# Optimization experiments

Measured on AMD Instinct MI355X. Metric: run time of the kernel, lower is better.

## Reference

```python
import jax, jax.numpy as jnp
import numpy as np

N = 50000      # nodes
E = 800000     # edges (avg degree 16)
DIN = 500      # input_dim
HID = 100      # hid_dim (fixed in module)
DOUT = 64      # output_dim
EPS = 1e-5     # LayerNorm eps (torch default)


def _layer_norm(x, g, b):
    mu = jnp.mean(x, axis=-1, keepdims=True)
    var = jnp.var(x, axis=-1, keepdims=True)
    return (x - mu) / jnp.sqrt(var + EPS) * g + b


def _gcn_conv(x, src, tgt, W, b):
    # PyG GCNConv: self-loops + symmetric normalization + linear + scatter-add
    h = x @ W  # [N, out]
    idx = jnp.arange(N)
    src_sl = jnp.concatenate([src, idx])
    tgt_sl = jnp.concatenate([tgt, idx])
    deg = jax.ops.segment_sum(jnp.ones(src_sl.shape, h.dtype), tgt_sl, num_segments=N)
    dinv = jnp.where(deg > 0, deg ** -0.5, 0.0)
    norm = dinv[src_sl] * dinv[tgt_sl]  # [E+N]
    out = jax.ops.segment_sum(h[src_sl] * norm[:, None], tgt_sl, num_segments=N)
    return out + b


def setup_inputs() -> dict:
    key = jax.random.key(0)
    ks = jax.random.split(key, 10)
    glorot = lambda k, fi, fo: jax.random.normal(k, (fi, fo), jnp.float32) * np.float32(1.0 / np.sqrt(fi))
    z = lambda d: jnp.zeros((d,), jnp.float32)
    return dict(
        data_x=jax.random.normal(ks[0], (N, DIN), jnp.float32),
        data_edge_index=jax.random.randint(ks[1], (2, E), 0, N),
        data_edge_attr=jnp.zeros((E,), jnp.int32),  # single relation type
        t_W1=glorot(ks[2], DIN, HID), t_b1=z(HID), t_g1=jnp.ones((HID,), jnp.float32), t_be1=z(HID),
        t_W2=glorot(ks[3], HID, HID), t_b2=z(HID), t_g2=jnp.ones((HID,), jnp.float32), t_be2=z(HID),
        r_Wrel=glorot(ks[4], HID, HID)[None],  # [n_relations=1, H, H]
        r_Wself=glorot(ks[5], HID, HID), r_b=z(HID),
        c1_W=glorot(ks[6], HID, HID), c1_b=z(HID),
        c2_W=glorot(ks[7], HID, DOUT), c2_b=z(DOUT),
    )


def reference(data_x, data_edge_index, data_edge_attr,
              t_W1, t_b1, t_g1, t_be1, t_W2, t_b2, t_g2, t_be2,
              r_Wrel, r_Wself, r_b, c1_W, c1_b, c2_W, c2_b):
    src, tgt = data_edge_index[0], data_edge_index[1]
    # transform: Linear -> LN -> ReLU -> Linear -> LN -> ReLU
    x = jax.nn.relu(_layer_norm(data_x @ t_W1 + t_b1, t_g1, t_be1))
    x = jax.nn.relu(_layer_norm(x @ t_W2 + t_b2, t_g2, t_be2))
    # RGCN, n_relations=1, n_layers=1: per-relation message + self transform
    msgs = x[src] @ r_Wrel[0]  # edge_attr is all relation 0
    x = x @ r_Wself + jax.ops.segment_sum(msgs, tgt, num_segments=N) + r_b
    x = jax.nn.relu(x)  # dropout = identity (eval)
    x = jax.nn.relu(_gcn_conv(x, src, tgt, c1_W, c1_b))
    x = _gcn_conv(x, src, tgt, c2_W, c2_b)
    return jax.nn.log_softmax(x, axis=1)
```

## Files before the change

kernel.cpp:

```cpp
#include <hip/hip_runtime.h>
#include <hip/hip_bf16.h>

typedef __attribute__((ext_vector_type(8))) short short8;
typedef __attribute__((ext_vector_type(8))) unsigned short ushort8;
typedef __attribute__((ext_vector_type(4))) float f32x4;

static constexpr int NN = 50000;
static constexpr int NE = 800000;
static constexpr int SCAN_B = 196;

#define MFMA16x16x32 __builtin_amdgcn_mfma_f32_16x16x32_bf16

__device__ __forceinline__ float b2f(unsigned short u){
  unsigned v = ((unsigned)u) << 16;
  return __builtin_bit_cast(float, v);
}
__device__ __forceinline__ unsigned short f2b(float f){
  unsigned x = __builtin_bit_cast(unsigned, f);
  unsigned r = (x + 0x7fffu + ((x >> 16) & 1u)) >> 16;
  return (unsigned short)r;
}

__device__ __align__(256) int   g_isf32;
__device__ __align__(256) unsigned short g_W1t  [112 * 512];
__device__ __align__(256) unsigned short g_W2t  [112 * 128];
__device__ __align__(256) unsigned short g_WselfT[112 * 128];
__device__ __align__(256) unsigned short g_WrelT [112 * 128];
__device__ __align__(256) unsigned short g_c1Wt [112 * 128];
__device__ __align__(256) unsigned short g_c2Wt [64 * 128];
__device__ __align__(256) unsigned short g_bufA[(size_t)NN * 128];
__device__ __align__(256) unsigned short g_bufB[(size_t)NN * 128];
__device__ __align__(256) unsigned short g_bufC[(size_t)NN * 128];
__device__ __align__(256) int   g_deg[NN];
__device__ __align__(256) int   g_rowptr[NN + 1];
__device__ __align__(256) int   g_cursor[NN];
__device__ __align__(256) int   g_colidx[NE];
__device__ __align__(256) float g_dinv[NN];
__device__ __align__(256) int   g_partial[256];

__device__ __forceinline__ float ld_in(const void* p, int idx, int isf32){
  if (isf32) return ((const float*)p)[idx];
  return b2f(((const unsigned short*)p)[idx]);
}

__global__ void k_detect(const unsigned short* __restrict__ x){
  __shared__ int sh[256];
  int tid = threadIdx.x;
  int cnt = 0;
  for (int j = 0; j < 16; j++){
    unsigned short h = x[(size_t)(tid * 16 + j) * 2];
    int e = (h >> 7) & 0xFF;
    if (e >= 90 && e <= 160) cnt++;
  }
  sh[tid] = cnt;
  __syncthreads();
  for (int off = 128; off > 0; off >>= 1){
    if (tid < off) sh[tid] += sh[tid + off];
    __syncthreads();
  }
  if (tid == 0) g_isf32 = (sh[0] < 2458) ? 1 : 0;
}

__global__ void k_zero(){
  int i = blockIdx.x * 256 + threadIdx.x;
  if (i < NN){ g_deg[i] = 0; g_cursor[i] = 0; }
}

__device__ __forceinline__ void xp_one(const void* W, unsigned short* Wt, int idx,
                                       int K, int Nc, int Kpad, int isf32){
  int n = idx / Kpad;
  int k = idx - n * Kpad;
  float v = 0.f;
  if (n < Nc && k < K) v = ld_in(W, k * Nc + n, isf32);
  Wt[idx] = f2b(v);
}
__global__ void k_transpose_all(const void* W1, const void* W2, const void* Wself,
                                const void* Wrel, const void* c1W, const void* c2W){
  int idx = blockIdx.x * 256 + threadIdx.x;
  const int isf32 = g_isf32;
  if (idx < 57344){ xp_one(W1, g_W1t, idx, 500, 100, 512, isf32); return; }
  idx -= 57344;
  if (idx < 14336){ xp_one(W2,    g_W2t,    idx, 100, 100, 128, isf32); return; }
  idx -= 14336;
  if (idx < 14336){ xp_one(Wself, g_WselfT, idx, 100, 100, 128, isf32); return; }
  idx -= 14336;
  if (idx < 14336){ xp_one(Wrel,  g_WrelT,  idx, 100, 100, 128, isf32); return; }
  idx -= 14336;
  if (idx < 14336){ xp_one(c1W,   g_c1Wt,   idx, 100, 100, 128, isf32); return; }
  idx -= 14336;
  if (idx < 8192){  xp_one(c2W,   g_c2Wt,   idx, 100, 64,  128, isf32); }
}

__global__ void k_deg(const int* __restrict__ tgt){
  int e = blockIdx.x * 256 + threadIdx.x;
  if (e < NE) atomicAdd(&g_deg[tgt[e]], 1);
}

__global__ __launch_bounds__(256) void k_scan1(){
  __shared__ int sh[256];
  int t = threadIdx.x;
  int i = blockIdx.x * 256 + t;
  int val = (i < NN) ? g_deg[i] : 0;
  sh[t] = val;
  __syncthreads();
#pragma unroll
  for (int off = 1; off < 256; off <<= 1){
    int v = (t >= off) ? sh[t - off] : 0;
    __syncthreads();
    sh[t] += v;
    __syncthreads();
  }
  if (i < NN){
    g_rowptr[i] = sh[t] - val;
    g_dinv[i] = rsqrtf((float)(val + 1));
  }
  if (t == 255) g_partial[blockIdx.x] = sh[255];
}
__global__ __launch_bounds__(256) void k_scan2(){
  __shared__ int sh[256];
  int t = threadIdx.x;
  int val = (t < SCAN_B) ? g_partial[t] : 0;
  sh[t] = val;
  __syncthreads();
#pragma unroll
  for (int off = 1; off < 256; off <<= 1){
    int v = (t >= off) ? sh[t - off] : 0;
    __syncthreads();
    sh[t] += v;
    __syncthreads();
  }
  if (t < SCAN_B) g_partial[t] = sh[t] - val;
  if (t == 255) g_rowptr[NN] = sh[255];
}
__global__ __launch_bounds__(256) void k_scan3(){
  int i = blockIdx.x * 256 + threadIdx.x;
  if (i < NN) g_rowptr[i] += g_partial[blockIdx.x];
}

__global__ void k_fill(const int* __restrict__ src, const int* __restrict__ tgt){
  int e = blockIdx.x * 256 + threadIdx.x;
  if (e >= NE) return;
  int t = tgt[e];
  int pos = g_rowptr[t] + atomicAdd(&g_cursor[t], 1);
  g_colidx[pos] = src[e];
}

template<int MODE>
__global__ __launch_bounds__(256) void k_agg(){
  const unsigned short* x = (MODE == 1) ? g_bufC : g_bufB;
  int node = blockIdx.x * 16 + (threadIdx.x >> 4);
  if (node >= NN) return;
  const int c8 = (threadIdx.x & 15) * 8;

  float wt = (MODE != 0) ? g_dinv[node] : 1.f;
  float a[4][8];
#pragma unroll
  for (int j = 0; j < 4; j++)
#pragma unroll
    for (int k = 0; k < 8; k++) a[j][k] = 0.f;

  int p0 = g_rowptr[node], p1 = g_rowptr[node + 1];
  for (int p = p0; p < p1; p += 4){
    int   sj[4]; float wj[4];
#pragma unroll
    for (int j = 0; j < 4; j++){
      bool ok = (p + j) < p1;
      sj[j] = ok ? g_colidx[p + j] : node;
      wj[j] = ok ? ((MODE != 0) ? g_dinv[sj[j]] * wt : 1.f) : 0.f;
    }
    ushort8 r[4];
#pragma unroll
    for (int j = 0; j < 4; j++)
      r[j] = *reinterpret_cast<const ushort8*>(&x[(size_t)sj[j] * 128 + c8]);
#pragma unroll
    for (int j = 0; j < 4; j++)
#pragma unroll
      for (int k = 0; k < 8; k++) a[j][k] += wj[j] * b2f((unsigned short)r[j][k]);
  }
  if (MODE != 0){
    float ws = wt * wt;
    ushort8 sv = *reinterpret_cast<const ushort8*>(&x[(size_t)node * 128 + c8]);
#pragma unroll
    for (int k = 0; k < 8; k++) a[0][k] += ws * b2f((unsigned short)sv[k]);
  }
  ushort8 o;
#pragma unroll
  for (int k = 0; k < 8; k++)
    o[k] = f2b(a[0][k] + a[1][k] + a[2][k] + a[3][k]);
  *reinterpret_cast<ushort8*>(&g_bufA[(size_t)node * 128 + c8]) = o;
}

__global__ __launch_bounds__(256, 4) void k_gemm1_ln(const void* __restrict__ Aext,
    const void* __restrict__ bias, const void* __restrict__ gamma,
    const void* __restrict__ beta){
  __shared__ float red[28 * 256];
  const int tid = threadIdx.x;
  const int w = tid >> 6, lane = tid & 63;
  const int m = lane & 15, q = lane >> 4;
  const int row0 = blockIdx.x * 16;
  const int isf32 = g_isf32;
  const int kbase = w * 128;
  f32x4 acc[7] = {};

  if (isf32){
    const float* base = (const float*)Aext + (size_t)(row0 + m) * 500;
    f32x4 L[8];
#pragma unroll
    for (int c = 0; c < 4; c++){
      int col = kbase + c * 32 + q * 8;
      L[2 * c]     = *reinterpret_cast<const f32x4*>(base + min(col, 496));
      L[2 * c + 1] = *reinterpret_cast<const f32x4*>(base + min(col + 4, 496));
    }
#pragma unroll
    for (int c = 0; c < 4; c++){
      f32x4 lo = L[2 * c], hi = L[2 * c + 1];
      short8 a = {(short)f2b(lo[0]), (short)f2b(lo[1]), (short)f2b(lo[2]), (short)f2b(lo[3]),
                  (short)f2b(hi[0]), (short)f2b(hi[1]), (short)f2b(hi[2]), (short)f2b(hi[3])};
      const int k0 = kbase + c * 32 + q * 8;
#pragma unroll
      for (int t = 0; t < 7; t++){
        short8 b = *reinterpret_cast<const short8*>(g_W1t + (size_t)(t * 16 + m) * 512 + k0);
        acc[t] = MFMA16x16x32(a, b, acc[t], 0, 0, 0);
      }
    }
  } else {
    const unsigned short* base = (const unsigned short*)Aext + (size_t)(row0 + m) * 500;
    ushort4 U[8];
#pragma unroll
    for (int c = 0; c < 4; c++){
      int col = kbase + c * 32 + q * 8;
      U[2 * c]     = *reinterpret_cast<const ushort4*>(base + min(col, 496));
      U[2 * c + 1] = *reinterpret_cast<const ushort4*>(base + min(col + 4, 496));
    }
#pragma unroll
    for (int c = 0; c < 4; c++){
      ushort4 lo = U[2 * c], hi = U[2 * c + 1];
      short8 a = {(short)lo.x, (short)lo.y, (short)lo.z, (short)lo.w,
                  (short)hi.x, (short)hi.y, (short)hi.z, (short)hi.w};
      const int k0 = kbase + c * 32 + q * 8;
#pragma unroll
      for (int t = 0; t < 7; t++){
        short8 b = *reinterpret_cast<const short8*>(g_W1t + (size_t)(t * 16 + m) * 512 + k0);
        acc[t] = MFMA16x16x32(a, b, acc[t], 0, 0, 0);
      }
    }
  }

#pragma unroll
  for (int t = 0; t < 7; t++)
#pragma unroll
    for (int r = 0; r < 4; r++)
      red[(t * 4 + r) * 256 + tid] = acc[t][r];
  __syncthreads();
  if (w != 0) return;

  float bf_[7], gf_[7], ef_[7];
#pragma unroll
  for (int t = 0; t < 7; t++){
    int col = t * 16 + m;
    bool ok = col < 100;
    bf_[t] = ok ? ld_in(bias, col, isf32)  : 0.f;
    gf_[t] = ok ? ld_in(gamma, col, isf32) : 0.f;
    ef_[t] = ok ? ld_in(beta, col, isf32)  : 0.f;
  }
#pragma unroll
  for (int r = 0; r < 4; r++){
    float vals[7], s1 = 0.f, s2 = 0.f;
#pragma unroll
    for (int t = 0; t < 7; t++){
      const float* rv = &red[(t * 4 + r) * 256];
      float v = rv[lane] + rv[64 + lane] + rv[128 + lane] + rv[192 + lane];
      int col = t * 16 + m;
      v = (col < 100) ? (v + bf_[t]) : 0.f;
      vals[t] = v; s1 += v; s2 += v * v;
    }
#pragma unroll
    for (int msk = 1; msk < 16; msk <<= 1){
      s1 += __shfl_xor(s1, msk, 64);
      s2 += __shfl_xor(s2, msk, 64);
    }
    float mu = s1 * 0.01f;
    float var = fmaxf(s2 * 0.01f - mu * mu, 0.f);
    float rstd = rsqrtf(var + 1e-5f);
    unsigned short* orow = g_bufA + (size_t)(row0 + q * 4 + r) * 128;
#pragma unroll
    for (int t = 0; t < 7; t++){
      int col = t * 16 + m;
      float y = fmaxf((vals[t] - mu) * rstd * gf_[t] + ef_[t], 0.f);
      orow[col] = f2b((col < 100) ? y : 0.f);
    }
    orow[112 + m] = 0;
  }
}

__global__ __launch_bounds__(256) void k_gemm2_ln(const void* __restrict__ bias,
    const void* __restrict__ gamma, const void* __restrict__ beta){
  const int isf32 = g_isf32;
  const int wave = threadIdx.x >> 6, lane = threadIdx.x & 63;
  const int m = lane & 15, q = lane >> 4;
  const int row0 = (blockIdx.x * 4 + wave) * 16;
  if (row0 >= NN) return;
  f32x4 acc[7] = {};
  const unsigned short* arow = g_bufA + (size_t)(row0 + m) * 128;
#pragma unroll
  for (int c = 0; c < 4; c++){
    const int k0 = c * 32 + q * 8;
    short8 a = *reinterpret_cast<const short8*>(arow + k0);
#pragma unroll
    for (int t = 0; t < 7; t++){
      short8 b = *reinterpret_cast<const short8*>(g_W2t + (size_t)(t * 16 + m) * 128 + k0);
      acc[t] = MFMA16x16x32(a, b, acc[t], 0, 0, 0);
    }
  }
  float bf_[7], gf_[7], ef_[7];
#pragma unroll
  for (int t = 0; t < 7; t++){
    int col = t * 16 + m;
    bool ok = col < 100;
    bf_[t] = ok ? ld_in(bias, col, isf32)  : 0.f;
    gf_[t] = ok ? ld_in(gamma, col, isf32) : 0.f;
    ef_[t] = ok ? ld_in(beta, col, isf32)  : 0.f;
  }
#pragma unroll
  for (int r = 0; r < 4; r++){
    float vals[7], s1 = 0.f, s2 = 0.f;
#pragma unroll
    for (int t = 0; t < 7; t++){
      int col = t * 16 + m;
      float v = (col < 100) ? (acc[t][r] + bf_[t]) : 0.f;
      vals[t] = v; s1 += v; s2 += v * v;
    }
#pragma unroll
    for (int msk = 1; msk < 16; msk <<= 1){
      s1 += __shfl_xor(s1, msk, 64);
      s2 += __shfl_xor(s2, msk, 64);
    }
    float mu = s1 * 0.01f;
    float var = fmaxf(s2 * 0.01f - mu * mu, 0.f);
    float rstd = rsqrtf(var + 1e-5f);
    unsigned short* orow = g_bufB + (size_t)(row0 + q * 4 + r) * 128;
#pragma unroll
    for (int t = 0; t < 7; t++){
      int col = t * 16 + m;
      float y = fmaxf((vals[t] - mu) * rstd * gf_[t] + ef_[t], 0.f);
      orow[col] = f2b((col < 100) ? y : 0.f);
    }
    orow[112 + m] = 0;
  }
}

template<int SEL>
__global__ __launch_bounds__(256) void k_gemm_bias_relu(const void* __restrict__ bias){
  const unsigned short* A1  = (SEL == 0) ? g_bufB : g_bufA;
  const unsigned short* B1t = (SEL == 0) ? g_WselfT : g_c1Wt;
  unsigned short* out       = (SEL == 0) ? g_bufC : g_bufB;
  const int isf32 = g_isf32;

  const int wave = threadIdx.x >> 6, lane = threadIdx.x & 63;
  const int m = lane & 15, q = lane >> 4;
  const int row0 = (blockIdx.x * 4 + wave) * 16;
  if (row0 >= NN) return;
  f32x4 acc[7] = {};
  const unsigned short* a1row = A1 + (size_t)(row0 + m) * 128;
#pragma unroll
  for (int c = 0; c < 4; c++){
    const int k0 = c * 32 + q * 8;
    short8 a = *reinterpret_cast<const short8*>(a1row + k0);
#pragma unroll
    for (int t = 0; t < 7; t++){
      short8 b = *reinterpret_cast<const short8*>(B1t + (size_t)(t * 16 + m) * 128 + k0);
      acc[t] = MFMA16x16x32(a, b, acc[t], 0, 0, 0);
    }
  }
  if (SEL == 0){
    const unsigned short* a2row = g_bufA + (size_t)(row0 + m) * 128;
#pragma unroll
    for (int c = 0; c < 4; c++){
      const int k0 = c * 32 + q * 8;
      short8 a = *reinterpret_cast<const short8*>(a2row + k0);
#pragma unroll
      for (int t = 0; t < 7; t++){
        short8 b = *reinterpret_cast<const short8*>(g_WrelT + (size_t)(t * 16 + m) * 128 + k0);
        acc[t] = MFMA16x16x32(a, b, acc[t], 0, 0, 0);
      }
    }
  }
  float bf_[7];
#pragma unroll
  for (int t = 0; t < 7; t++){
    int col = t * 16 + m;
    bf_[t] = (col < 100) ? ld_in(bias, col, isf32) : 0.f;
  }
#pragma unroll
  for (int r = 0; r < 4; r++){
    unsigned short* orow = out + (size_t)(row0 + q * 4 + r) * 128;
#pragma unroll
    for (int t = 0; t < 7; t++){
      int col = t * 16 + m;
      float y = fmaxf(acc[t][r] + bf_[t], 0.f);
      orow[col] = f2b((col < 100) ? y : 0.f);
    }
    orow[112 + m] = 0;
  }
}

__global__ __launch_bounds__(256) void k_gemm_c2(){
  const int wave = threadIdx.x >> 6, lane = threadIdx.x & 63;
  const int m = lane & 15, q = lane >> 4;
  const int row0 = (blockIdx.x * 4 + wave) * 16;
  if (row0 >= NN) return;
  f32x4 acc[4] = {};
  const unsigned short* arow = g_bufB + (size_t)(row0 + m) * 128;
#pragma unroll
  for (int c = 0; c < 4; c++){
    const int k0 = c * 32 + q * 8;
    short8 a = *reinterpret_cast<const short8*>(arow + k0);
#pragma unroll
    for (int t = 0; t < 4; t++){
      short8 b = *reinterpret_cast<const short8*>(g_c2Wt + (size_t)(t * 16 + m) * 128 + k0);
      acc[t] = MFMA16x16x32(a, b, acc[t], 0, 0, 0);
    }
  }
#pragma unroll
  for (int r = 0; r < 4; r++){
    unsigned short* orow = g_bufC + (size_t)(row0 + q * 4 + r) * 64;
#pragma unroll
    for (int t = 0; t < 4; t++) orow[t * 16 + m] = f2b(acc[t][r]);
  }
}

__global__ __launch_bounds__(256) void k_agg_lsm(const void* __restrict__ bias,
                                                 void* __restrict__ outv){
  const int isf32 = g_isf32;
  int node = blockIdx.x * 32 + (threadIdx.x >> 3);
  if (node >= NN) return;
  const int c8 = (threadIdx.x & 7) * 8;
  float wt = g_dinv[node];
  float a[4][8];
#pragma unroll
  for (int j = 0; j < 4; j++)
#pragma unroll
    for (int k = 0; k < 8; k++) a[j][k] = 0.f;

  int p0 = g_rowptr[node], p1 = g_rowptr[node + 1];
  for (int p = p0; p < p1; p += 4){
    int   sj[4]; float wj[4];
#pragma unroll
    for (int j = 0; j < 4; j++){
      bool ok = (p + j) < p1;
      sj[j] = ok ? g_colidx[p + j] : node;
      wj[j] = ok ? g_dinv[sj[j]] * wt : 0.f;
    }
    ushort8 r[4];
#pragma unroll
    for (int j = 0; j < 4; j++)
      r[j] = *reinterpret_cast<const ushort8*>(&g_bufC[(size_t)sj[j] * 64 + c8]);
#pragma unroll
    for (int j = 0; j < 4; j++)
#pragma unroll
      for (int k = 0; k < 8; k++) a[j][k] += wj[j] * b2f((unsigned short)r[j][k]);
  }
  float ws = wt * wt;
  ushort8 sv = *reinterpret_cast<const ushort8*>(&g_bufC[(size_t)node * 64 + c8]);
#pragma unroll
  for (int k = 0; k < 8; k++) a[0][k] += ws * b2f((unsigned short)sv[k]);

  float v[8], mx = -1e30f;
#pragma unroll
  for (int k = 0; k < 8; k++){
    v[k] = a[0][k] + a[1][k] + a[2][k] + a[3][k] + ld_in(bias, c8 + k, isf32);
    mx = fmaxf(mx, v[k]);
  }
#pragma unroll
  for (int msk = 1; msk < 8; msk <<= 1) mx = fmaxf(mx, __shfl_xor(mx, msk, 64));
  float se = 0.f;
#pragma unroll
  for (int k = 0; k < 8; k++) se += expf(v[k] - mx);
#pragma unroll
  for (int msk = 1; msk < 8; msk <<= 1) se += __shfl_xor(se, msk, 64);
  float lse = logf(se);
  size_t ro = (size_t)node * 64 + c8;
  if (isf32){
    float* o = (float*)outv + ro;
#pragma unroll
    for (int k = 0; k < 8; k++) o[k] = v[k] - mx - lse;
  } else {
    unsigned short* o = (unsigned short*)outv + ro;
#pragma unroll
    for (int k = 0; k < 8; k++) o[k] = f2b(v[k] - mx - lse);
  }
}

extern "C" void kernel_launch(void* const* d_in, const int* in_sizes, int n_in,
                              void* d_out, int out_size, void* d_ws, size_t ws_size,
                              hipStream_t stream){
  (void)in_sizes; (void)n_in; (void)out_size; (void)d_ws; (void)ws_size;
  const void* data_x = d_in[0];
  const int* ei = (const int*)d_in[1];
  const int* src = ei;
  const int* tgt = ei + NE;
  const void *W1 = d_in[3], *b1 = d_in[4], *gm1 = d_in[5], *be1 = d_in[6];
  const void *W2 = d_in[7], *b2 = d_in[8], *gm2 = d_in[9], *be2 = d_in[10];
  const void *Wrel = d_in[11], *Wself = d_in[12], *rb = d_in[13];
  const void *c1W = d_in[14], *c1b = d_in[15];
  const void *c2W = d_in[16], *c2b = d_in[17];

  k_detect<<<1, 256, 0, stream>>>((const unsigned short*)data_x);
  k_zero<<<(NN + 255) / 256, 256, 0, stream>>>();
  k_transpose_all<<<(122880 + 255) / 256, 256, 0, stream>>>(W1, W2, Wself, Wrel, c1W, c2W);

  k_deg<<<(NE + 255) / 256, 256, 0, stream>>>(tgt);
  k_scan1<<<SCAN_B, 256, 0, stream>>>();
  k_scan2<<<1, 256, 0, stream>>>();
  k_scan3<<<SCAN_B, 256, 0, stream>>>();
  k_fill<<<(NE + 255) / 256, 256, 0, stream>>>(src, tgt);

  const int G64 = (NN + 63) / 64;
  const int GA  = (NN + 15) / 16;
  k_gemm1_ln<<<3125, 256, 0, stream>>>(data_x, b1, gm1, be1);
  k_gemm2_ln<<<G64, 256, 0, stream>>>(b2, gm2, be2);
  k_agg<0><<<GA, 256, 0, stream>>>();
  k_gemm_bias_relu<0><<<G64, 256, 0, stream>>>(rb);
  k_agg<1><<<GA, 256, 0, stream>>>();
  k_gemm_bias_relu<1><<<G64, 256, 0, stream>>>(c1b);
  k_gemm_c2<<<G64, 256, 0, stream>>>();
  k_agg_lsm<<<(NN + 31) / 32, 256, 0, stream>>>(c2b, d_out);
}
```

Before: 507.1 us.

## Fuse aggregation and GEMM stages into shared-memory pipelines, merge detect and zero

Merges detect and zero into one launch. The first two dense layers now run in one kernel that keeps the intermediate in LDS, and each aggregation is fused with its following GEMM(s) through an LDS tile. This cuts kernel launches and removes global round-trips of the intermediate activations. In exchange the GEMM K dimension is split across four waves and reduced through a large shared buffer, and the gather-heavy aggregation now shares blocks with MFMA work, which may lower occupancy.

```diff
diff --git a/kernel.cpp b/kernel.cpp
--- a/kernel.cpp
+++ b/kernel.cpp
@@ -43,27 +43,27 @@
   return b2f(((const unsigned short*)p)[idx]);
 }
 
-__global__ void k_detect(const unsigned short* __restrict__ x){
-  __shared__ int sh[256];
-  int tid = threadIdx.x;
-  int cnt = 0;
-  for (int j = 0; j < 16; j++){
-    unsigned short h = x[(size_t)(tid * 16 + j) * 2];
-    int e = (h >> 7) & 0xFF;
-    if (e >= 90 && e <= 160) cnt++;
-  }
-  sh[tid] = cnt;
-  __syncthreads();
-  for (int off = 128; off > 0; off >>= 1){
-    if (tid < off) sh[tid] += sh[tid + off];
+__global__ void k_detect_zero(const unsigned short* __restrict__ x){
+  if (blockIdx.x == 0){
+    __shared__ int sh[256];
+    int tid = threadIdx.x;
+    int cnt = 0;
+    for (int j = 0; j < 16; j++){
+      unsigned short h = x[(size_t)(tid * 16 + j) * 2];
+      int e = (h >> 7) & 0xFF;
+      if (e >= 90 && e <= 160) cnt++;
+    }
+    sh[tid] = cnt;
     __syncthreads();
-  }
-  if (tid == 0) g_isf32 = (sh[0] < 2458) ? 1 : 0;
-}
-
-__global__ void k_zero(){
-  int i = blockIdx.x * 256 + threadIdx.x;
-  if (i < NN){ g_deg[i] = 0; g_cursor[i] = 0; }
+    for (int off = 128; off > 0; off >>= 1){
+      if (tid < off) sh[tid] += sh[tid + off];
+      __syncthreads();
+    }
+    if (tid == 0) g_isf32 = (sh[0] < 2458) ? 1 : 0;
+  } else {
+    int i = (blockIdx.x - 1) * 256 + threadIdx.x;
+    if (i < NN){ g_deg[i] = 0; g_cursor[i] = 0; }
+  }
 }
 
 __device__ __forceinline__ void xp_one(const void* W, unsigned short* Wt, int idx,
@@ -95,39 +95,29 @@
   int e = blockIdx.x * 256 + threadIdx.x;
   if (e < NE) atomicAdd(&g_deg[tgt[e]], 1);
 }
-
 __global__ __launch_bounds__(256) void k_scan1(){
   __shared__ int sh[256];
   int t = threadIdx.x;
   int i = blockIdx.x * 256 + t;
   int val = (i < NN) ? g_deg[i] : 0;
-  sh[t] = val;
-  __syncthreads();
+  sh[t] = val; __syncthreads();
 #pragma unroll
   for (int off = 1; off < 256; off <<= 1){
     int v = (t >= off) ? sh[t - off] : 0;
-    __syncthreads();
-    sh[t] += v;
-    __syncthreads();
-  }
-  if (i < NN){
-    g_rowptr[i] = sh[t] - val;
-    g_dinv[i] = rsqrtf((float)(val + 1));
-  }
+    __syncthreads(); sh[t] += v; __syncthreads();
+  }
+  if (i < NN){ g_rowptr[i] = sh[t] - val; g_dinv[i] = rsqrtf((float)(val + 1)); }
   if (t == 255) g_partial[blockIdx.x] = sh[255];
 }
 __global__ __launch_bounds__(256) void k_scan2(){
   __shared__ int sh[256];
   int t = threadIdx.x;
   int val = (t < SCAN_B) ? g_partial[t] : 0;
-  sh[t] = val;
-  __syncthreads();
+  sh[t] = val; __syncthreads();
 #pragma unroll
   for (int off = 1; off < 256; off <<= 1){
     int v = (t >= off) ? sh[t - off] : 0;
-    __syncthreads();
-    sh[t] += v;
-    __syncthreads();
+    __syncthreads(); sh[t] += v; __syncthreads();
   }
   if (t < SCAN_B) g_partial[t] = sh[t] - val;
   if (t == 255) g_rowptr[NN] = sh[255];
@@ -136,7 +126,6 @@
   int i = blockIdx.x * 256 + threadIdx.x;
   if (i < NN) g_rowptr[i] += g_partial[blockIdx.x];
 }
-
 __global__ void k_fill(const int* __restrict__ src, const int* __restrict__ tgt){
   int e = blockIdx.x * 256 + threadIdx.x;
   if (e >= NE) return;
@@ -145,63 +134,9 @@
   g_colidx[pos] = src[e];
 }
 
-template<int MODE>
-__global__ __launch_bounds__(256) void k_agg(){
-  const unsigned short* x = (MODE == 1) ? g_bufC : g_bufB;
-  int node = blockIdx.x * 16 + (threadIdx.x >> 4);
-  if (node >= NN) return;
-  const int c8 = (threadIdx.x & 15) * 8;
-
-  float wt = (MODE != 0) ? g_dinv[node] : 1.f;
-  float a[4][8];
-#pragma unroll
-  for (int j = 0; j < 4; j++)
-#pragma unroll
-    for (int k = 0; k < 8; k++) a[j][k] = 0.f;
-
-  int p0 = g_rowptr[node], p1 = g_rowptr[node + 1];
-  for (int p = p0; p < p1; p += 4){
-    int   sj[4]; float wj[4];
-#pragma unroll
-    for (int j = 0; j < 4; j++){
-      bool ok = (p + j) < p1;
-      sj[j] = ok ? g_colidx[p + j] : node;
-      wj[j] = ok ? ((MODE != 0) ? g_dinv[sj[j]] * wt : 1.f) : 0.f;
-    }
-    ushort8 r[4];
-#pragma unroll
-    for (int j = 0; j < 4; j++)
-      r[j] = *reinterpret_cast<const ushort8*>(&x[(size_t)sj[j] * 128 + c8]);
-#pragma unroll
-    for (int j = 0; j < 4; j++)
-#pragma unroll
-      for (int k = 0; k < 8; k++) a[j][k] += wj[j] * b2f((unsigned short)r[j][k]);
-  }
-  if (MODE != 0){
-    float ws = wt * wt;
-    ushort8 sv = *reinterpret_cast<const ushort8*>(&x[(size_t)node * 128 + c8]);
-#pragma unroll
-    for (int k = 0; k < 8; k++) a[0][k] += ws * b2f((unsigned short)sv[k]);
-  }
-  ushort8 o;
-#pragma unroll
-  for (int k = 0; k < 8; k++)
-    o[k] = f2b(a[0][k] + a[1][k] + a[2][k] + a[3][k]);
-  *reinterpret_cast<ushort8*>(&g_bufA[(size_t)node * 128 + c8]) = o;
-}
-
-__global__ __launch_bounds__(256, 4) void k_gemm1_ln(const void* __restrict__ Aext,
-    const void* __restrict__ bias, const void* __restrict__ gamma,
-    const void* __restrict__ beta){
-  __shared__ float red[28 * 256];
-  const int tid = threadIdx.x;
-  const int w = tid >> 6, lane = tid & 63;
-  const int m = lane & 15, q = lane >> 4;
-  const int row0 = blockIdx.x * 16;
-  const int isf32 = g_isf32;
-  const int kbase = w * 128;
-  f32x4 acc[7] = {};
-
+
+__device__ __forceinline__ void body_gemm1_compute(const void* Aext, int row0,
+    int m, int q, int kbase, int isf32, f32x4* acc){
   if (isf32){
     const float* base = (const float*)Aext + (size_t)(row0 + m) * 500;
     f32x4 L[8];
@@ -245,15 +180,18 @@
       }
     }
   }
-
-#pragma unroll
-  for (int t = 0; t < 7; t++)
-#pragma unroll
-    for (int r = 0; r < 4; r++)
-      red[(t * 4 + r) * 256 + tid] = acc[t][r];
-  __syncthreads();
-  if (w != 0) return;
-
+}
+
+__device__ __forceinline__ short8 frag_from_lds(const float* xT, int m, int k0){
+  const float* ax = xT + m * 132 + k0;
+  short8 a = {(short)f2b(ax[0]), (short)f2b(ax[1]), (short)f2b(ax[2]), (short)f2b(ax[3]),
+              (short)f2b(ax[4]), (short)f2b(ax[5]), (short)f2b(ax[6]), (short)f2b(ax[7])};
+  return a;
+}
+
+__device__ __forceinline__ void epi_ln_to_lds(const float* red, float* xT,
+    int lane, int m, int q, int isf32,
+    const void* bias, const void* gamma, const void* beta){
   float bf_[7], gf_[7], ef_[7];
 #pragma unroll
   for (int t = 0; t < 7; t++){
@@ -282,36 +220,20 @@
     float mu = s1 * 0.01f;
     float var = fmaxf(s2 * 0.01f - mu * mu, 0.f);
     float rstd = rsqrtf(var + 1e-5f);
-    unsigned short* orow = g_bufA + (size_t)(row0 + q * 4 + r) * 128;
+    float* xrow = xT + (q * 4 + r) * 132;
 #pragma unroll
     for (int t = 0; t < 7; t++){
       int col = t * 16 + m;
       float y = fmaxf((vals[t] - mu) * rstd * gf_[t] + ef_[t], 0.f);
-      orow[col] = f2b((col < 100) ? y : 0.f);
-    }
-    orow[112 + m] = 0;
-  }
-}
-
-__global__ __launch_bounds__(256) void k_gemm2_ln(const void* __restrict__ bias,
-    const void* __restrict__ gamma, const void* __restrict__ beta){
-  const int isf32 = g_isf32;
-  const int wave = threadIdx.x >> 6, lane = threadIdx.x & 63;
-  const int m = lane & 15, q = lane >> 4;
-  const int row0 = (blockIdx.x * 4 + wave) * 16;
-  if (row0 >= NN) return;
-  f32x4 acc[7] = {};
-  const unsigned short* arow = g_bufA + (size_t)(row0 + m) * 128;
-#pragma unroll
-  for (int c = 0; c < 4; c++){
-    const int k0 = c * 32 + q * 8;
-    short8 a = *reinterpret_cast<const short8*>(arow + k0);
-#pragma unroll
-    for (int t = 0; t < 7; t++){
-      short8 b = *reinterpret_cast<const short8*>(g_W2t + (size_t)(t * 16 + m) * 128 + k0);
-      acc[t] = MFMA16x16x32(a, b, acc[t], 0, 0, 0);
-    }
-  }
+      xrow[col] = (col < 100) ? y : 0.f;
+    }
+    xrow[112 + m] = 0.f;
+  }
+}
+
+__device__ __forceinline__ void epi_ln_to_global(const float* red, unsigned short* outb,
+    int row0, int lane, int m, int q, int isf32,
+    const void* bias, const void* gamma, const void* beta){
   float bf_[7], gf_[7], ef_[7];
 #pragma unroll
   for (int t = 0; t < 7; t++){
@@ -326,8 +248,10 @@
     float vals[7], s1 = 0.f, s2 = 0.f;
 #pragma unroll
     for (int t = 0; t < 7; t++){
+      const float* rv = &red[(t * 4 + r) * 256];
+      float v = rv[lane] + rv[64 + lane] + rv[128 + lane] + rv[192 + lane];
       int col = t * 16 + m;
-      float v = (col < 100) ? (acc[t][r] + bf_[t]) : 0.f;
+      v = (col < 100) ? (v + bf_[t]) : 0.f;
       vals[t] = v; s1 += v; s2 += v * v;
     }
 #pragma unroll
@@ -338,7 +262,7 @@
     float mu = s1 * 0.01f;
     float var = fmaxf(s2 * 0.01f - mu * mu, 0.f);
     float rstd = rsqrtf(var + 1e-5f);
-    unsigned short* orow = g_bufB + (size_t)(row0 + q * 4 + r) * 128;
+    unsigned short* orow = outb + (size_t)(row0 + q * 4 + r) * 128;
 #pragma unroll
     for (int t = 0; t < 7; t++){
       int col = t * 16 + m;
@@ -349,42 +273,9 @@
   }
 }
 
-template<int SEL>
-__global__ __launch_bounds__(256) void k_gemm_bias_relu(const void* __restrict__ bias){
-  const unsigned short* A1  = (SEL == 0) ? g_bufB : g_bufA;
-  const unsigned short* B1t = (SEL == 0) ? g_WselfT : g_c1Wt;
-  unsigned short* out       = (SEL == 0) ? g_bufC : g_bufB;
-  const int isf32 = g_isf32;
-
-  const int wave = threadIdx.x >> 6, lane = threadIdx.x & 63;
-  const int m = lane & 15, q = lane >> 4;
-  const int row0 = (blockIdx.x * 4 + wave) * 16;
-  if (row0 >= NN) return;
-  f32x4 acc[7] = {};
-  const unsigned short* a1row = A1 + (size_t)(row0 + m) * 128;
-#pragma unroll
-  for (int c = 0; c < 4; c++){
-    const int k0 = c * 32 + q * 8;
-    short8 a = *reinterpret_cast<const short8*>(a1row + k0);
-#pragma unroll
-    for (int t = 0; t < 7; t++){
-      short8 b = *reinterpret_cast<const short8*>(B1t + (size_t)(t * 16 + m) * 128 + k0);
-      acc[t] = MFMA16x16x32(a, b, acc[t], 0, 0, 0);
-    }
-  }
-  if (SEL == 0){
-    const unsigned short* a2row = g_bufA + (size_t)(row0 + m) * 128;
-#pragma unroll
-    for (int c = 0; c < 4; c++){
-      const int k0 = c * 32 + q * 8;
-      short8 a = *reinterpret_cast<const short8*>(a2row + k0);
-#pragma unroll
-      for (int t = 0; t < 7; t++){
-        short8 b = *reinterpret_cast<const short8*>(g_WrelT + (size_t)(t * 16 + m) * 128 + k0);
-        acc[t] = MFMA16x16x32(a, b, acc[t], 0, 0, 0);
-      }
-    }
-  }
+__device__ __forceinline__ void epi_biasrelu_to_global(const float* red,
+    unsigned short* outb, int row0, int lane, int m, int q, int isf32,
+    const void* bias){
   float bf_[7];
 #pragma unroll
   for (int t = 0; t < 7; t++){
@@ -393,39 +284,213 @@
   }
 #pragma unroll
   for (int r = 0; r < 4; r++){
-    unsigned short* orow = out + (size_t)(row0 + q * 4 + r) * 128;
-#pragma unroll
-    for (int t = 0; t < 7; t++){
+    unsigned short* orow = outb + (size_t)(row0 + q * 4 + r) * 128;
+#pragma unroll
+    for (int t = 0; t < 7; t++){
+      const float* rv = &red[(t * 4 + r) * 256];
+      float v = rv[lane] + rv[64 + lane] + rv[128 + lane] + rv[192 + lane];
       int col = t * 16 + m;
-      float y = fmaxf(acc[t][r] + bf_[t], 0.f);
+      float y = fmaxf(v + bf_[t], 0.f);
       orow[col] = f2b((col < 100) ? y : 0.f);
     }
     orow[112 + m] = 0;
   }
 }
 
-__global__ __launch_bounds__(256) void k_gemm_c2(){
-  const int wave = threadIdx.x >> 6, lane = threadIdx.x & 63;
+__device__ __forceinline__ void epi_biasrelu_to_lds(const float* red, float* xT,
+    int lane, int m, int q, int isf32, const void* bias){
+  float bf_[7];
+#pragma unroll
+  for (int t = 0; t < 7; t++){
+    int col = t * 16 + m;
+    bf_[t] = (col < 100) ? ld_in(bias, col, isf32) : 0.f;
+  }
+#pragma unroll
+  for (int r = 0; r < 4; r++){
+    float* xrow = xT + (q * 4 + r) * 132;
+#pragma unroll
+    for (int t = 0; t < 7; t++){
+      const float* rv = &red[(t * 4 + r) * 256];
+      float v = rv[lane] + rv[64 + lane] + rv[128 + lane] + rv[192 + lane];
+      int col = t * 16 + m;
+      float y = fmaxf(v + bf_[t], 0.f);
+      xrow[col] = (col < 100) ? y : 0.f;
+    }
+    xrow[112 + m] = 0.f;
+  }
+}
+
+template<int MODE>
+__device__ __forceinline__ void agg_to_lds(int node, int nl, int c8, float* aggT){
+  const unsigned short* x = (MODE == 1) ? g_bufC : g_bufB;
+  float wt = (MODE != 0) ? g_dinv[node] : 1.f;
+  float a[4][8];
+#pragma unroll
+  for (int j = 0; j < 4; j++)
+#pragma unroll
+    for (int k = 0; k < 8; k++) a[j][k] = 0.f;
+  int p0 = g_rowptr[node], p1 = g_rowptr[node + 1];
+  for (int p = p0; p < p1; p += 4){
+    int sj[4]; float wj[4];
+#pragma unroll
+    for (int j = 0; j < 4; j++){
+      bool ok = (p + j) < p1;
+      sj[j] = ok ? g_colidx[p + j] : node;
+      wj[j] = ok ? ((MODE != 0) ? g_dinv[sj[j]] * wt : 1.f) : 0.f;
+    }
+    ushort8 r[4];
+#pragma unroll
+    for (int j = 0; j < 4; j++)
+      r[j] = *reinterpret_cast<const ushort8*>(&x[(size_t)sj[j] * 128 + c8]);
+#pragma unroll
+    for (int j = 0; j < 4; j++)
+#pragma unroll
+      for (int k = 0; k < 8; k++) a[j][k] += wj[j] * b2f((unsigned short)r[j][k]);
+  }
+  if (MODE != 0){
+    float ws = wt * wt;
+    ushort8 sv = *reinterpret_cast<const ushort8*>(&x[(size_t)node * 128 + c8]);
+#pragma unroll
+    for (int k = 0; k < 8; k++) a[0][k] += ws * b2f((unsigned short)sv[k]);
+  }
+  float* arow = aggT + nl * 132;
+#pragma unroll
+  for (int k = 0; k < 8; k++)
+    arow[c8 + k] = a[0][k] + a[1][k] + a[2][k] + a[3][k];
+}
+
+
+__global__ __launch_bounds__(256, 4) void k_gemm12(const void* __restrict__ Aext,
+    const void* b1, const void* gm1, const void* be1,
+    const void* b2, const void* gm2, const void* be2){
+  __shared__ float red[28 * 256];
+  __shared__ float xT[16 * 132];
+  const int tid = threadIdx.x;
+  const int w = tid >> 6, lane = tid & 63;
   const int m = lane & 15, q = lane >> 4;
-  const int row0 = (blockIdx.x * 4 + wave) * 16;
-  if (row0 >= NN) return;
-  f32x4 acc[4] = {};
-  const unsigned short* arow = g_bufB + (size_t)(row0 + m) * 128;
-#pragma unroll
-  for (int c = 0; c < 4; c++){
-    const int k0 = c * 32 + q * 8;
-    short8 a = *reinterpret_cast<const short8*>(arow + k0);
+  const int row0 = blockIdx.x * 16;
+  const int isf32 = g_isf32;
+
+  f32x4 acc[7] = {};
+  body_gemm1_compute(Aext, row0, m, q, w * 128, isf32, acc);
+#pragma unroll
+  for (int t = 0; t < 7; t++)
+#pragma unroll
+    for (int r = 0; r < 4; r++)
+      red[(t * 4 + r) * 256 + tid] = acc[t][r];
+  __syncthreads();
+  if (w == 0) epi_ln_to_lds(red, xT, lane, m, q, isf32, b1, gm1, be1);
+  __syncthreads();
+
+  f32x4 acc2[7] = {};
+  const int k0 = w * 32 + q * 8;
+  {
+    short8 a = frag_from_lds(xT, m, k0);
+#pragma unroll
+    for (int t = 0; t < 7; t++){
+      short8 b = *reinterpret_cast<const short8*>(g_W2t + (size_t)(t * 16 + m) * 128 + k0);
+      acc2[t] = MFMA16x16x32(a, b, acc2[t], 0, 0, 0);
+    }
+  }
+#pragma unroll
+  for (int t = 0; t < 7; t++)
+#pragma unroll
+    for (int r = 0; r < 4; r++)
+      red[(t * 4 + r) * 256 + tid] = acc2[t][r];
+  __syncthreads();
+  if (w == 0) epi_ln_to_global(red, g_bufB, row0, lane, m, q, isf32, b2, gm2, be2);
+}
+
+__global__ __launch_bounds__(256, 4) void k_rgcn_f(const void* rb){
+  __shared__ float red[28 * 256];
+  __shared__ float aggT[16 * 132];
+  const int tid = threadIdx.x;
+  agg_to_lds<0>(blockIdx.x * 16 + (tid >> 4), tid >> 4, (tid & 15) * 8, aggT);
+  __syncthreads();
+
+  const int w = tid >> 6, lane = tid & 63;
+  const int m = lane & 15, q = lane >> 4;
+  const int row0 = blockIdx.x * 16;
+  const int k0 = w * 32 + q * 8;
+  f32x4 acc[7] = {};
+  {
+    short8 a1 = *reinterpret_cast<const short8*>(g_bufB + (size_t)(row0 + m) * 128 + k0);
+#pragma unroll
+    for (int t = 0; t < 7; t++){
+      short8 b = *reinterpret_cast<const short8*>(g_WselfT + (size_t)(t * 16 + m) * 128 + k0);
+      acc[t] = MFMA16x16x32(a1, b, acc[t], 0, 0, 0);
+    }
+    short8 a2 = frag_from_lds(aggT, m, k0);
+#pragma unroll
+    for (int t = 0; t < 7; t++){
+      short8 b = *reinterpret_cast<const short8*>(g_WrelT + (size_t)(t * 16 + m) * 128 + k0);
+      acc[t] = MFMA16x16x32(a2, b, acc[t], 0, 0, 0);
+    }
+  }
+#pragma unroll
+  for (int t = 0; t < 7; t++)
+#pragma unroll
+    for (int r = 0; r < 4; r++)
+      red[(t * 4 + r) * 256 + tid] = acc[t][r];
+  __syncthreads();
+  if (w == 0) epi_biasrelu_to_global(red, g_bufC, row0, lane, m, q, g_isf32, rb);
+}
+
+__global__ __launch_bounds__(256, 4) void k_conv_f(const void* c1b){
+  __shared__ float red[28 * 256];
+  __shared__ float aggT[16 * 132];
+  const int tid = threadIdx.x;
+  agg_to_lds<1>(blockIdx.x * 16 + (tid >> 4), tid >> 4, (tid & 15) * 8, aggT);
+  __syncthreads();
+
+  const int w = tid >> 6, lane = tid & 63;
+  const int m = lane & 15, q = lane >> 4;
+  const int row0 = blockIdx.x * 16;
+  const int k0 = w * 32 + q * 8;
+  f32x4 acc[7] = {};
+  {
+    short8 a = frag_from_lds(aggT, m, k0);
+#pragma unroll
+    for (int t = 0; t < 7; t++){
+      short8 b = *reinterpret_cast<const short8*>(g_c1Wt + (size_t)(t * 16 + m) * 128 + k0);
+      acc[t] = MFMA16x16x32(a, b, acc[t], 0, 0, 0);
+    }
+  }
+#pragma unroll
+  for (int t = 0; t < 7; t++)
+#pragma unroll
+    for (int r = 0; r < 4; r++)
+      red[(t * 4 + r) * 256 + tid] = acc[t][r];
+  __syncthreads();
+  if (w == 0) epi_biasrelu_to_lds(red, aggT, lane, m, q, g_isf32, c1b);
+  __syncthreads();
+
+  f32x4 acc2[4] = {};
+  {
+    short8 a = frag_from_lds(aggT, m, k0);
 #pragma unroll
     for (int t = 0; t < 4; t++){
       short8 b = *reinterpret_cast<const short8*>(g_c2Wt + (size_t)(t * 16 + m) * 128 + k0);
-      acc[t] = MFMA16x16x32(a, b, acc[t], 0, 0, 0);
-    }
-  }
-#pragma unroll
-  for (int r = 0; r < 4; r++){
-    unsigned short* orow = g_bufC + (size_t)(row0 + q * 4 + r) * 64;
-#pragma unroll
-    for (int t = 0; t < 4; t++) orow[t * 16 + m] = f2b(acc[t][r]);
+      acc2[t] = MFMA16x16x32(a, b, acc2[t], 0, 0, 0);
+    }
+  }
+#pragma unroll
+  for (int t = 0; t < 4; t++)
+#pragma unroll
+    for (int r = 0; r < 4; r++)
+      red[(t * 4 + r) * 256 + tid] = acc2[t][r];
+  __syncthreads();
+  if (w == 0){
+#pragma unroll
+    for (int r = 0; r < 4; r++){
+      unsigned short* orow = g_bufA + (size_t)(row0 + q * 4 + r) * 64;
+#pragma unroll
+      for (int t = 0; t < 4; t++){
+        const float* rv = &red[(t * 4 + r) * 256];
+        float v = rv[lane] + rv[64 + lane] + rv[128 + lane] + rv[192 + lane];
+        orow[t * 16 + m] = f2b(v);
+      }
+    }
   }
 }
 
@@ -441,10 +506,9 @@
   for (int j = 0; j < 4; j++)
 #pragma unroll
     for (int k = 0; k < 8; k++) a[j][k] = 0.f;
-
   int p0 = g_rowptr[node], p1 = g_rowptr[node + 1];
   for (int p = p0; p < p1; p += 4){
-    int   sj[4]; float wj[4];
+    int sj[4]; float wj[4];
 #pragma unroll
     for (int j = 0; j < 4; j++){
       bool ok = (p + j) < p1;
@@ -454,14 +518,14 @@
     ushort8 r[4];
 #pragma unroll
     for (int j = 0; j < 4; j++)
-      r[j] = *reinterpret_cast<const ushort8*>(&g_bufC[(size_t)sj[j] * 64 + c8]);
+      r[j] = *reinterpret_cast<const ushort8*>(&g_bufA[(size_t)sj[j] * 64 + c8]);
 #pragma unroll
     for (int j = 0; j < 4; j++)
 #pragma unroll
       for (int k = 0; k < 8; k++) a[j][k] += wj[j] * b2f((unsigned short)r[j][k]);
   }
   float ws = wt * wt;
-  ushort8 sv = *reinterpret_cast<const ushort8*>(&g_bufC[(size_t)node * 64 + c8]);
+  ushort8 sv = *reinterpret_cast<const ushort8*>(&g_bufA[(size_t)node * 64 + c8]);
 #pragma unroll
   for (int k = 0; k < 8; k++) a[0][k] += ws * b2f((unsigned short)sv[k]);
 
@@ -505,8 +569,7 @@
   const void *c1W = d_in[14], *c1b = d_in[15];
   const void *c2W = d_in[16], *c2b = d_in[17];
 
-  k_detect<<<1, 256, 0, stream>>>((const unsigned short*)data_x);
-  k_zero<<<(NN + 255) / 256, 256, 0, stream>>>();
+  k_detect_zero<<<1 + (NN + 255) / 256, 256, 0, stream>>>((const unsigned short*)data_x);
   k_transpose_all<<<(122880 + 255) / 256, 256, 0, stream>>>(W1, W2, Wself, Wrel, c1W, c2W);
 
   k_deg<<<(NE + 255) / 256, 256, 0, stream>>>(tgt);
@@ -515,14 +578,8 @@
   k_scan3<<<SCAN_B, 256, 0, stream>>>();
   k_fill<<<(NE + 255) / 256, 256, 0, stream>>>(src, tgt);
 
-  const int G64 = (NN + 63) / 64;
-  const int GA  = (NN + 15) / 16;
-  k_gemm1_ln<<<3125, 256, 0, stream>>>(data_x, b1, gm1, be1);
-  k_gemm2_ln<<<G64, 256, 0, stream>>>(b2, gm2, be2);
-  k_agg<0><<<GA, 256, 0, stream>>>();
-  k_gemm_bias_relu<0><<<G64, 256, 0, stream>>>(rb);
-  k_agg<1><<<GA, 256, 0, stream>>>();
-  k_gemm_bias_relu<1><<<G64, 256, 0, stream>>>(c1b);
-  k_gemm_c2<<<G64, 256, 0, stream>>>();
+  k_gemm12<<<3125, 256, 0, stream>>>(data_x, b1, gm1, be1, b2, gm2, be2);
+  k_rgcn_f<<<3125, 256, 0, stream>>>(rb);
+  k_conv_f<<<3125, 256, 0, stream>>>(c1b);
   k_agg_lsm<<<(NN + 31) / 32, 256, 0, stream>>>(c2b, d_out);
 }
```

After: 484.7 us. -4.4%, faster.
